# Optimization experiments

Measured on AMD Instinct MI355X. Metric: run time of the kernel, lower is better.

## Reference

```python
import jax, jax.numpy as jnp
import numpy as np

N = 50000      # nodes
E = 800000     # edges (avg degree 16)
D_IN = 128     # in_feats
D_OUT = 128    # out_feats
EPS = 1e-5     # LayerNorm eps


def setup_inputs() -> dict:
    key = jax.random.key(0)
    ks = jax.random.split(key, 8)
    stdv = 1.0 / np.sqrt(5 * D_IN)
    return {
        "h": jax.random.normal(ks[0], (N, D_IN), dtype=jnp.float32),
        "dist": jax.random.uniform(ks[1], (E,), dtype=jnp.float32),
        "W": jax.random.uniform(ks[2], (D_OUT, 5 * D_IN), minval=-stdv, maxval=stdv, dtype=jnp.float32),
        "b": jax.random.uniform(ks[3], (D_OUT,), minval=-stdv, maxval=stdv, dtype=jnp.float32),
        "gamma": jnp.ones((D_OUT,), dtype=jnp.float32),
        "beta": jnp.zeros((D_OUT,), dtype=jnp.float32),
        "src": jax.random.randint(ks[4], (E,), 0, N, dtype=jnp.int32),
        "dst": jax.random.randint(ks[5], (E,), 0, N, dtype=jnp.int32),
        "positions": jax.random.randint(ks[6], (E,), 0, 4, dtype=jnp.int32),
    }


def reference(h, dist, W, b, gamma, beta, src, dst, positions):
    n = h.shape[0]
    h_src = h[src]  # [E, D] gather once, reused by all four directions

    def direction(p):
        # edge-masked u_mul_e + sum aggregation to dst
        w = jnp.where(positions == p, dist, 0.0)
        return jax.ops.segment_sum(h_src * w[:, None], dst, num_segments=n)

    r = direction(0)   # right
    bt = direction(1)  # bottom
    l = direction(2)   # left
    t = direction(0)   # top (original code reuses positions == 0 — faithful)

    cat = jnp.concatenate([h, r, bt, l, t], axis=1)  # [N, 5D]
    z = cat @ W.T + b                                 # [N, D_OUT]
    mu = jnp.mean(z, axis=-1, keepdims=True)
    var = jnp.mean(jnp.square(z - mu), axis=-1, keepdims=True)
    z = (z - mu) * jax.lax.rsqrt(var + EPS) * gamma + beta
    return jax.nn.relu(z)
```

## Files before the change

kernel.cpp:

```cpp
#include <hip/hip_runtime.h>
#include <math.h>
#include <stdint.h>

constexpr int NN = 50000;
constexpr int EE = 800000;
constexpr int D  = 128;
constexpr int KK = 512;
constexpr int BM = 32;
constexpr int CAP = 64;
constexpr int NBLK = (NN + BM - 1) / BM;

typedef __attribute__((ext_vector_type(8)))  short bf16x8;
typedef __attribute__((ext_vector_type(16))) float f32x16;

__device__ inline unsigned short f2bf(float x) {
    unsigned u = __builtin_bit_cast(unsigned, x);
    unsigned r = (u + 0x7FFF + ((u >> 16) & 1)) >> 16;
    return (unsigned short)r;
}
__device__ inline float bf2f(unsigned short b) {
    unsigned u = ((unsigned)b) << 16;
    return __builtin_bit_cast(float, u);
}

__global__ __launch_bounds__(256) void prep_wfrag(const float* __restrict__ W,
                                                  unsigned short* __restrict__ Wfh,
                                                  unsigned short* __restrict__ Wfl)
{
    int tid = blockIdx.x * 256 + threadIdx.x;
    int ln  = tid & 31;
    int slot = (tid >> 5) & 63;
    int cb  = tid >> 11;
    int col = cb * 32 + ln;
    short h8[8], l8[8];
#pragma unroll
    for (int j = 0; j < 8; ++j) {
        int k = slot * 8 + j;
        float v = W[col * 640 + k];
        if (k >= 128 && k < 256) v += W[col * 640 + k + 384];
        unsigned short hb = f2bf(v);
        h8[j] = (short)hb;
        l8[j] = (short)f2bf(v - bf2f(hb));
    }
    *(bf16x8*)(Wfh + (size_t)tid * 8) = *(bf16x8*)h8;
    *(bf16x8*)(Wfl + (size_t)tid * 8) = *(bf16x8*)l8;
}

__global__ __launch_bounds__(256) void fill_bucket(const int* __restrict__ src,
                                                   const int* __restrict__ dst,
                                                   const int* __restrict__ pos,
                                                   const float* __restrict__ dist,
                                                   int* __restrict__ deg,
                                                   int2* __restrict__ bucket)
{
    int e = blockIdx.x * 256 + threadIdx.x;
    if (e >= EE) return;
    int p = pos[e];
    if (p == 3) return;
    int d_ = dst[e];
    int slot = atomicAdd(&deg[d_], 1);
    if (slot < CAP)
        bucket[(size_t)d_ * CAP + slot] =
            make_int2(src[e] | (p << 16), __float_as_int(dist[e]));
}

__global__ __launch_bounds__(256, 4) void fused_agg_gemm(
    const float* __restrict__ h,
    const int2* __restrict__ bucket, const int* __restrict__ deg,
    const unsigned short* __restrict__ Wfh, const unsigned short* __restrict__ Wfl,
    const float* __restrict__ bias, const float* __restrict__ gamma,
    const float* __restrict__ beta, float* __restrict__ out)
{
    __shared__ __align__(16) short Af[64 * 32 * 8];

    const int t = threadIdx.x;
    const int lane = t & 63;
    const int w = t >> 6;
    const int ln = lane & 31;
    const int hs = lane >> 5;
    const int node0 = blockIdx.x * BM;

    {
        int row = t >> 3;
        int g   = t & 7;
        int node = node0 + row;
        float ff[16];
        if (node < NN) {
            const float* hp = h + (size_t)node * D + g * 16;
            float4 f0 = *(const float4*)hp;
            float4 f1 = *(const float4*)(hp + 4);
            float4 f2 = *(const float4*)(hp + 8);
            float4 f3 = *(const float4*)(hp + 12);
            ff[0]=f0.x; ff[1]=f0.y; ff[2]=f0.z; ff[3]=f0.w;
            ff[4]=f1.x; ff[5]=f1.y; ff[6]=f1.z; ff[7]=f1.w;
            ff[8]=f2.x; ff[9]=f2.y; ff[10]=f2.z; ff[11]=f2.w;
            ff[12]=f3.x; ff[13]=f3.y; ff[14]=f3.z; ff[15]=f3.w;
        } else {
#pragma unroll
            for (int j = 0; j < 16; ++j) ff[j] = 0.f;
        }
        short b16[16];
#pragma unroll
        for (int j = 0; j < 16; ++j) b16[j] = (short)f2bf(ff[j]);
        int s0 = 2 * g, s1 = 2 * g + 1;
        *(bf16x8*)(Af + (s0 * 32 + (row ^ s0)) * 8) = *(bf16x8*)&b16[0];
        *(bf16x8*)(Af + (s1 * 32 + (row ^ s1)) * 8) = *(bf16x8*)&b16[8];
    }

    const int c0 = ln * 4;
    for (int i = 0; i < 8; ++i) {
        int r = w * 8 + i;
        int node = node0 + r;
        int n = 0;
        if (node < NN) {
            n = deg[node];
            if (n > CAP) n = CAP;
        }
        int2 mreg = (lane < n) ? bucket[(size_t)node * CAP + lane]
                               : make_int2(0, 0);

        float a0[4] = {0.f, 0.f, 0.f, 0.f};
        float a1[4] = {0.f, 0.f, 0.f, 0.f};
        float a2[4] = {0.f, 0.f, 0.f, 0.f};

        for (int base = 0; base < n; base += 16) {
            float4 v[8];
            float  wq[8];
            int    pq[8];
#pragma unroll
            for (int j = 0; j < 8; ++j) {
                int idx = base + 2 * j + hs;
                bool pred = idx < n;
                int mx = __shfl(mreg.x, idx & 63, 64);
                int my = __shfl(mreg.y, idx & 63, 64);
                pq[j] = mx >> 16;
                wq[j] = pred ? __int_as_float(my) : 0.f;
                const float* hp = h + (size_t)(mx & 0xFFFF) * D + c0;
                v[j] = pred ? *(const float4*)hp : make_float4(0.f,0.f,0.f,0.f);
            }
#pragma unroll
            for (int j = 0; j < 8; ++j) {
                float w0 = (pq[j] == 0) ? wq[j] : 0.f;
                float w1 = (pq[j] == 1) ? wq[j] : 0.f;
                float w2 = (pq[j] == 2) ? wq[j] : 0.f;
                float vv[4] = {v[j].x, v[j].y, v[j].z, v[j].w};
#pragma unroll
                for (int c = 0; c < 4; ++c) {
                    a0[c] = fmaf(vv[c], w0, a0[c]);
                    a1[c] = fmaf(vv[c], w1, a1[c]);
                    a2[c] = fmaf(vv[c], w2, a2[c]);
                }
            }
        }
#pragma unroll
        for (int c = 0; c < 4; ++c) {
            a0[c] += __shfl_xor(a0[c], 32, 64);
            a1[c] += __shfl_xor(a1[c], 32, 64);
            a2[c] += __shfl_xor(a2[c], 32, 64);
        }
        int sb = ln >> 1;
        int bo = (ln & 1) * 4;
        if (hs == 0) {
            uint2 u0 = make_uint2((unsigned)f2bf(a0[0]) | ((unsigned)f2bf(a0[1]) << 16),
                                  (unsigned)f2bf(a0[2]) | ((unsigned)f2bf(a0[3]) << 16));
            uint2 u1 = make_uint2((unsigned)f2bf(a1[0]) | ((unsigned)f2bf(a1[1]) << 16),
                                  (unsigned)f2bf(a1[2]) | ((unsigned)f2bf(a1[3]) << 16));
            int s = 16 + sb;
            *(uint2*)(Af + (s * 32 + (r ^ (s & 31))) * 8 + bo) = u0;
            s = 32 + sb;
            *(uint2*)(Af + (s * 32 + (r ^ (s & 31))) * 8 + bo) = u1;
        } else {
            uint2 u2 = make_uint2((unsigned)f2bf(a2[0]) | ((unsigned)f2bf(a2[1]) << 16),
                                  (unsigned)f2bf(a2[2]) | ((unsigned)f2bf(a2[3]) << 16));
            int s = 48 + sb;
            *(uint2*)(Af + (s * 32 + (r ^ (s & 31))) * 8 + bo) = u2;
        }
    }

    __syncthreads();

    f32x16 acc;
#pragma unroll
    for (int i = 0; i < 16; ++i) acc[i] = 0.f;

    auto LOADB = [&](int k16, bf16x8& bh, bf16x8& bl) {
        size_t fo = ((size_t)(w * 64 + k16 * 2 + hs) * 32 + ln) * 8;
        bh = *(const bf16x8*)(Wfh + fo);
        bl = *(const bf16x8*)(Wfl + fo);
    };
    auto LOADA = [&](int k16) -> bf16x8 {
        int s = k16 * 2 + hs;
        return *(const bf16x8*)(Af + (s * 32 + (ln ^ (s & 31))) * 8);
    };

    bf16x8 bh0, bl0, bh1, bl1;
    LOADB(0, bh0, bl0);
#pragma unroll
    for (int k16 = 0; k16 < 32; k16 += 2) {
        if (k16 + 1 < 32) LOADB(k16 + 1, bh1, bl1);
        bf16x8 aa = LOADA(k16);
        __builtin_amdgcn_s_setprio(1);
        acc = __builtin_amdgcn_mfma_f32_32x32x16_bf16(aa, bh0, acc, 0, 0, 0);
        acc = __builtin_amdgcn_mfma_f32_32x32x16_bf16(aa, bl0, acc, 0, 0, 0);
        __builtin_amdgcn_s_setprio(0);
        if (k16 + 2 < 32) LOADB(k16 + 2, bh0, bl0);
        aa = LOADA(k16 + 1);
        __builtin_amdgcn_s_setprio(1);
        acc = __builtin_amdgcn_mfma_f32_32x32x16_bf16(aa, bh1, acc, 0, 0, 0);
        acc = __builtin_amdgcn_mfma_f32_32x32x16_bf16(aa, bl1, acc, 0, 0, 0);
        __builtin_amdgcn_s_setprio(0);
    }

    __syncthreads();

    float* part = (float*)Af;
    float bias_c = bias[w * 32 + ln];

#pragma unroll
    for (int reg = 0; reg < 16; ++reg) {
        float z = acc[reg] + bias_c;
        acc[reg] = z;
        float s = z, ss = z * z;
#pragma unroll
        for (int m = 1; m < 32; m <<= 1) {
            s  += __shfl_xor(s, m, 64);
            ss += __shfl_xor(ss, m, 64);
        }
        int rl = (reg & 3) + 8 * (reg >> 2) + 4 * hs;
        if (ln == 0) {
            part[(w * 32 + rl) * 2]     = s;
            part[(w * 32 + rl) * 2 + 1] = ss;
        }
    }
    __syncthreads();

    float g_c  = gamma[w * 32 + ln];
    float be_c = beta[w * 32 + ln];
#pragma unroll
    for (int reg = 0; reg < 16; ++reg) {
        int rl = (reg & 3) + 8 * (reg >> 2) + 4 * hs;
        float s  = part[rl * 2]     + part[(32 + rl) * 2]
                 + part[(64 + rl) * 2] + part[(96 + rl) * 2];
        float ss = part[rl * 2 + 1] + part[(32 + rl) * 2 + 1]
                 + part[(64 + rl) * 2 + 1] + part[(96 + rl) * 2 + 1];
        float mu  = s * (1.f / 128.f);
        float var = ss * (1.f / 128.f) - mu * mu;
        float rs  = rsqrtf(var + 1e-5f);
        int grow = node0 + rl;
        if (grow < NN) {
            float v = (acc[reg] - mu) * rs * g_c + be_c;
            out[(size_t)grow * D + w * 32 + ln] = v > 0.f ? v : 0.f;
        }
    }
}

extern "C" void kernel_launch(void* const* d_in, const int* in_sizes, int n_in,
                              void* d_out, int out_size, void* d_ws, size_t ws_size,
                              hipStream_t stream)
{
    const float* h     = (const float*)d_in[0];
    const float* dist  = (const float*)d_in[1];
    const float* W     = (const float*)d_in[2];
    const float* bias  = (const float*)d_in[3];
    const float* gamma = (const float*)d_in[4];
    const float* beta  = (const float*)d_in[5];
    const int*   src   = (const int*)d_in[6];
    const int*   dst   = (const int*)d_in[7];
    const int*   pos   = (const int*)d_in[8];

    unsigned short* Wfh = (unsigned short*)d_ws;
    unsigned short* Wfl = Wfh + 128 * KK;
    int*  deg    = (int*)(Wfl + 128 * KK);
    int2* bucket = (int2*)(((uintptr_t)(deg + NN) + 15) & ~(uintptr_t)15);

    hipMemsetAsync(deg, 0, NN * sizeof(int), stream);

    prep_wfrag<<<32, 256, 0, stream>>>(W, Wfh, Wfl);
    fill_bucket<<<(EE + 255) / 256, 256, 0, stream>>>(src, dst, pos, dist, deg, bucket);
    fused_agg_gemm<<<NBLK, 256, 0, stream>>>(h, bucket, deg, Wfh, Wfl,
                                             bias, gamma, beta, (float*)d_out);
}
```

Before: 199.2 us.

## Reorder to transform-then-aggregate: project node features first, gather bf16 projections

Uses linearity to apply the per-direction weight slices to every node before aggregation: a GEMM computes the self term plus three 128-wide projections per node (stored as bf16 in Y), and a separate per-node kernel gathers the projected rows weighted by dist and applies LayerNorm/ReLU. Edge indices now encode src*3+p so each edge reads exactly one 128-wide bf16 row instead of a float row accumulated into three buffers, which halves gather bytes and cuts FMA work. In exchange it writes and rereads a 50000x384 bf16 intermediate plus a float base array, adds a kernel launch, and rounds the aggregated operand to bf16 before summation, which changes numerical error.

```diff
diff --git a/kernel.cpp b/kernel.cpp
--- a/kernel.cpp
+++ b/kernel.cpp
@@ -5,10 +5,9 @@
 constexpr int NN = 50000;
 constexpr int EE = 800000;
 constexpr int D  = 128;
-constexpr int KK = 512;
+constexpr int CAP = 64;
 constexpr int BM = 32;
-constexpr int CAP = 64;
-constexpr int NBLK = (NN + BM - 1) / BM;
+constexpr int NBX = (NN + BM - 1) / BM;
 
 typedef __attribute__((ext_vector_type(8)))  short bf16x8;
 typedef __attribute__((ext_vector_type(16))) float f32x16;
@@ -29,15 +28,20 @@
 {
     int tid = blockIdx.x * 256 + threadIdx.x;
     int ln  = tid & 31;
-    int slot = (tid >> 5) & 63;
-    int cb  = tid >> 11;
-    int col = cb * 32 + ln;
+    int hs  = (tid >> 5) & 1;
+    int s   = (tid >> 6) & 7;
+    int vcb = tid >> 9;
+    int oc  = vcb * 32 + ln;
     short h8[8], l8[8];
 #pragma unroll
     for (int j = 0; j < 8; ++j) {
-        int k = slot * 8 + j;
-        float v = W[col * 640 + k];
-        if (k >= 128 && k < 256) v += W[col * 640 + k + 384];
+        int k = s * 16 + hs * 8 + j;
+        float v;
+        if (oc < 128)      v = W[oc * 640 + k];
+        else if (oc < 256) v = W[(oc - 128) * 640 + 128 + k]
+                             + W[(oc - 128) * 640 + 512 + k];
+        else if (oc < 384) v = W[(oc - 256) * 640 + 256 + k];
+        else               v = W[(oc - 384) * 640 + 384 + k];
         unsigned short hb = f2bf(v);
         h8[j] = (short)hb;
         l8[j] = (short)f2bf(v - bf2f(hb));
@@ -61,17 +65,16 @@
     int slot = atomicAdd(&deg[d_], 1);
     if (slot < CAP)
         bucket[(size_t)d_ * CAP + slot] =
-            make_int2(src[e] | (p << 16), __float_as_int(dist[e]));
-}
-
-__global__ __launch_bounds__(256, 4) void fused_agg_gemm(
+            make_int2(src[e] * 3 + p, __float_as_int(dist[e]));
+}
+
+__global__ __launch_bounds__(256, 4) void pre_gemm(
     const float* __restrict__ h,
-    const int2* __restrict__ bucket, const int* __restrict__ deg,
     const unsigned short* __restrict__ Wfh, const unsigned short* __restrict__ Wfl,
-    const float* __restrict__ bias, const float* __restrict__ gamma,
-    const float* __restrict__ beta, float* __restrict__ out)
-{
-    __shared__ __align__(16) short Af[64 * 32 * 8];
+    const float* __restrict__ bias,
+    float* __restrict__ base, unsigned short* __restrict__ Y)
+{
+    __shared__ __align__(16) short Af[16 * 32 * 8];
 
     const int t = threadIdx.x;
     const int lane = t & 63;
@@ -79,6 +82,7 @@
     const int ln = lane & 31;
     const int hs = lane >> 5;
     const int node0 = blockIdx.x * BM;
+    const int by = blockIdx.y;
 
     {
         int row = t >> 3;
@@ -106,151 +110,121 @@
         *(bf16x8*)(Af + (s0 * 32 + (row ^ s0)) * 8) = *(bf16x8*)&b16[0];
         *(bf16x8*)(Af + (s1 * 32 + (row ^ s1)) * 8) = *(bf16x8*)&b16[8];
     }
-
-    const int c0 = ln * 4;
-    for (int i = 0; i < 8; ++i) {
-        int r = w * 8 + i;
-        int node = node0 + r;
-        int n = 0;
-        if (node < NN) {
-            n = deg[node];
-            if (n > CAP) n = CAP;
-        }
-        int2 mreg = (lane < n) ? bucket[(size_t)node * CAP + lane]
-                               : make_int2(0, 0);
-
-        float a0[4] = {0.f, 0.f, 0.f, 0.f};
-        float a1[4] = {0.f, 0.f, 0.f, 0.f};
-        float a2[4] = {0.f, 0.f, 0.f, 0.f};
-
-        for (int base = 0; base < n; base += 16) {
-            float4 v[8];
-            float  wq[8];
-            int    pq[8];
-#pragma unroll
-            for (int j = 0; j < 8; ++j) {
-                int idx = base + 2 * j + hs;
-                bool pred = idx < n;
-                int mx = __shfl(mreg.x, idx & 63, 64);
-                int my = __shfl(mreg.y, idx & 63, 64);
-                pq[j] = mx >> 16;
-                wq[j] = pred ? __int_as_float(my) : 0.f;
-                const float* hp = h + (size_t)(mx & 0xFFFF) * D + c0;
-                v[j] = pred ? *(const float4*)hp : make_float4(0.f,0.f,0.f,0.f);
-            }
-#pragma unroll
-            for (int j = 0; j < 8; ++j) {
-                float w0 = (pq[j] == 0) ? wq[j] : 0.f;
-                float w1 = (pq[j] == 1) ? wq[j] : 0.f;
-                float w2 = (pq[j] == 2) ? wq[j] : 0.f;
-                float vv[4] = {v[j].x, v[j].y, v[j].z, v[j].w};
-#pragma unroll
-                for (int c = 0; c < 4; ++c) {
-                    a0[c] = fmaf(vv[c], w0, a0[c]);
-                    a1[c] = fmaf(vv[c], w1, a1[c]);
-                    a2[c] = fmaf(vv[c], w2, a2[c]);
-                }
-            }
-        }
-#pragma unroll
-        for (int c = 0; c < 4; ++c) {
-            a0[c] += __shfl_xor(a0[c], 32, 64);
-            a1[c] += __shfl_xor(a1[c], 32, 64);
-            a2[c] += __shfl_xor(a2[c], 32, 64);
-        }
-        int sb = ln >> 1;
-        int bo = (ln & 1) * 4;
-        if (hs == 0) {
-            uint2 u0 = make_uint2((unsigned)f2bf(a0[0]) | ((unsigned)f2bf(a0[1]) << 16),
-                                  (unsigned)f2bf(a0[2]) | ((unsigned)f2bf(a0[3]) << 16));
-            uint2 u1 = make_uint2((unsigned)f2bf(a1[0]) | ((unsigned)f2bf(a1[1]) << 16),
-                                  (unsigned)f2bf(a1[2]) | ((unsigned)f2bf(a1[3]) << 16));
-            int s = 16 + sb;
-            *(uint2*)(Af + (s * 32 + (r ^ (s & 31))) * 8 + bo) = u0;
-            s = 32 + sb;
-            *(uint2*)(Af + (s * 32 + (r ^ (s & 31))) * 8 + bo) = u1;
-        } else {
-            uint2 u2 = make_uint2((unsigned)f2bf(a2[0]) | ((unsigned)f2bf(a2[1]) << 16),
-                                  (unsigned)f2bf(a2[2]) | ((unsigned)f2bf(a2[3]) << 16));
-            int s = 48 + sb;
-            *(uint2*)(Af + (s * 32 + (r ^ (s & 31))) * 8 + bo) = u2;
-        }
-    }
-
     __syncthreads();
 
-    f32x16 acc;
-#pragma unroll
-    for (int i = 0; i < 16; ++i) acc[i] = 0.f;
-
-    auto LOADB = [&](int k16, bf16x8& bh, bf16x8& bl) {
-        size_t fo = ((size_t)(w * 64 + k16 * 2 + hs) * 32 + ln) * 8;
+    const int vcb = by * 4 + w;
+
+    auto LOADB = [&](int s, bf16x8& bh, bf16x8& bl) {
+        size_t fo = ((size_t)((vcb * 8 + s) * 2 + hs) * 32 + ln) * 8;
         bh = *(const bf16x8*)(Wfh + fo);
         bl = *(const bf16x8*)(Wfl + fo);
     };
-    auto LOADA = [&](int k16) -> bf16x8 {
-        int s = k16 * 2 + hs;
-        return *(const bf16x8*)(Af + (s * 32 + (ln ^ (s & 31))) * 8);
+    auto LOADA = [&](int s) -> bf16x8 {
+        int sl = s * 2 + hs;
+        return *(const bf16x8*)(Af + (sl * 32 + (ln ^ sl)) * 8);
     };
+
+    f32x16 acc;
+#pragma unroll
+    for (int i = 0; i < 16; ++i) acc[i] = 0.f;
 
     bf16x8 bh0, bl0, bh1, bl1;
     LOADB(0, bh0, bl0);
 #pragma unroll
-    for (int k16 = 0; k16 < 32; k16 += 2) {
-        if (k16 + 1 < 32) LOADB(k16 + 1, bh1, bl1);
-        bf16x8 aa = LOADA(k16);
+    for (int s = 0; s < 8; s += 2) {
+        if (s + 1 < 8) LOADB(s + 1, bh1, bl1);
+        bf16x8 aa = LOADA(s);
         __builtin_amdgcn_s_setprio(1);
         acc = __builtin_amdgcn_mfma_f32_32x32x16_bf16(aa, bh0, acc, 0, 0, 0);
         acc = __builtin_amdgcn_mfma_f32_32x32x16_bf16(aa, bl0, acc, 0, 0, 0);
         __builtin_amdgcn_s_setprio(0);
-        if (k16 + 2 < 32) LOADB(k16 + 2, bh0, bl0);
-        aa = LOADA(k16 + 1);
+        if (s + 2 < 8) LOADB(s + 2, bh0, bl0);
+        aa = LOADA(s + 1);
         __builtin_amdgcn_s_setprio(1);
         acc = __builtin_amdgcn_mfma_f32_32x32x16_bf16(aa, bh1, acc, 0, 0, 0);
         acc = __builtin_amdgcn_mfma_f32_32x32x16_bf16(aa, bl1, acc, 0, 0, 0);
         __builtin_amdgcn_s_setprio(0);
     }
 
-    __syncthreads();
-
-    float* part = (float*)Af;
-    float bias_c = bias[w * 32 + ln];
-
-#pragma unroll
-    for (int reg = 0; reg < 16; ++reg) {
-        float z = acc[reg] + bias_c;
-        acc[reg] = z;
-        float s = z, ss = z * z;
-#pragma unroll
-        for (int m = 1; m < 32; m <<= 1) {
-            s  += __shfl_xor(s, m, 64);
-            ss += __shfl_xor(ss, m, 64);
-        }
-        int rl = (reg & 3) + 8 * (reg >> 2) + 4 * hs;
-        if (ln == 0) {
-            part[(w * 32 + rl) * 2]     = s;
-            part[(w * 32 + rl) * 2 + 1] = ss;
-        }
-    }
-    __syncthreads();
-
-    float g_c  = gamma[w * 32 + ln];
-    float be_c = beta[w * 32 + ln];
+    int vc = by * 128 + w * 32 + ln;
 #pragma unroll
     for (int reg = 0; reg < 16; ++reg) {
         int rl = (reg & 3) + 8 * (reg >> 2) + 4 * hs;
-        float s  = part[rl * 2]     + part[(32 + rl) * 2]
-                 + part[(64 + rl) * 2] + part[(96 + rl) * 2];
-        float ss = part[rl * 2 + 1] + part[(32 + rl) * 2 + 1]
-                 + part[(64 + rl) * 2 + 1] + part[(96 + rl) * 2 + 1];
-        float mu  = s * (1.f / 128.f);
-        float var = ss * (1.f / 128.f) - mu * mu;
-        float rs  = rsqrtf(var + 1e-5f);
         int grow = node0 + rl;
         if (grow < NN) {
-            float v = (acc[reg] - mu) * rs * g_c + be_c;
-            out[(size_t)grow * D + w * 32 + ln] = v > 0.f ? v : 0.f;
-        }
+            if (by == 0)
+                base[(size_t)grow * D + vc] = acc[reg] + bias[vc];
+            else
+                Y[(size_t)grow * 384 + (vc - 128)] = f2bf(acc[reg]);
+        }
+    }
+}
+
+__global__ __launch_bounds__(256, 8) void agg_ln(
+    const unsigned short* __restrict__ Y, const float* __restrict__ base,
+    const int2* __restrict__ bucket, const int* __restrict__ deg,
+    const float* __restrict__ gamma, const float* __restrict__ beta,
+    float* __restrict__ out)
+{
+    int w = threadIdx.x >> 6;
+    int node = blockIdx.x * 4 + w;
+    if (node >= NN) return;
+    int lane = threadIdx.x & 63;
+    int ln = lane & 31;
+    int hs = lane >> 5;
+
+    int n = deg[node];
+    if (n > CAP) n = CAP;
+    int2 mreg = (lane < n) ? bucket[(size_t)node * CAP + lane] : make_int2(0, 0);
+
+    float a[4] = {0.f, 0.f, 0.f, 0.f};
+    for (int b0 = 0; b0 < n; b0 += 16) {
+        ushort4 v[8];
+        float   wq[8];
+#pragma unroll
+        for (int j = 0; j < 8; ++j) {
+            int idx = b0 + 2 * j + hs;
+            int s3 = __shfl(mreg.x, idx, 64);
+            int wy = __shfl(mreg.y, idx, 64);
+            wq[j] = __int_as_float(wy);
+            v[j] = *(const ushort4*)(Y + (size_t)s3 * D + ln * 4);
+        }
+#pragma unroll
+        for (int j = 0; j < 8; ++j) {
+            a[0] = fmaf(bf2f(v[j].x), wq[j], a[0]);
+            a[1] = fmaf(bf2f(v[j].y), wq[j], a[1]);
+            a[2] = fmaf(bf2f(v[j].z), wq[j], a[2]);
+            a[3] = fmaf(bf2f(v[j].w), wq[j], a[3]);
+        }
+    }
+#pragma unroll
+    for (int c = 0; c < 4; ++c) a[c] += __shfl_xor(a[c], 32, 64);
+
+    float4 bv = *(const float4*)(base + (size_t)node * D + ln * 4);
+    float z[4] = {bv.x + a[0], bv.y + a[1], bv.z + a[2], bv.w + a[3]};
+
+    float s = z[0] + z[1] + z[2] + z[3];
+    float ss = z[0]*z[0] + z[1]*z[1] + z[2]*z[2] + z[3]*z[3];
+#pragma unroll
+    for (int m = 1; m < 32; m <<= 1) {
+        s  += __shfl_xor(s, m, 64);
+        ss += __shfl_xor(ss, m, 64);
+    }
+    float mu  = s * (1.f / 128.f);
+    float var = ss * (1.f / 128.f) - mu * mu;
+    float rs  = rsqrtf(var + 1e-5f);
+
+    if (hs == 0) {
+        float4 g4 = *(const float4*)(gamma + ln * 4);
+        float4 b4 = *(const float4*)(beta + ln * 4);
+        float o[4];
+        o[0] = (z[0] - mu) * rs * g4.x + b4.x;
+        o[1] = (z[1] - mu) * rs * g4.y + b4.y;
+        o[2] = (z[2] - mu) * rs * g4.z + b4.z;
+        o[3] = (z[3] - mu) * rs * g4.w + b4.w;
+#pragma unroll
+        for (int c = 0; c < 4; ++c) o[c] = o[c] > 0.f ? o[c] : 0.f;
+        *(float4*)(out + (size_t)node * D + ln * 4) = *(float4*)o;
     }
 }
 
@@ -268,15 +242,18 @@
     const int*   dst   = (const int*)d_in[7];
     const int*   pos   = (const int*)d_in[8];
 
-    unsigned short* Wfh = (unsigned short*)d_ws;
-    unsigned short* Wfl = Wfh + 128 * KK;
-    int*  deg    = (int*)(Wfl + 128 * KK);
+    unsigned short* Wfh  = (unsigned short*)d_ws;
+    unsigned short* Wfl  = Wfh + 8192 * 8;
+    unsigned short* Y    = Wfl + 8192 * 8;
+    float*          base = (float*)(Y + (size_t)NN * 384);
+    int*            deg  = (int*)(base + (size_t)NN * D);
     int2* bucket = (int2*)(((uintptr_t)(deg + NN) + 15) & ~(uintptr_t)15);
 
     hipMemsetAsync(deg, 0, NN * sizeof(int), stream);
 
     prep_wfrag<<<32, 256, 0, stream>>>(W, Wfh, Wfl);
     fill_bucket<<<(EE + 255) / 256, 256, 0, stream>>>(src, dst, pos, dist, deg, bucket);
-    fused_agg_gemm<<<NBLK, 256, 0, stream>>>(h, bucket, deg, Wfh, Wfl,
-                                             bias, gamma, beta, (float*)d_out);
-}
+    pre_gemm<<<dim3(NBX, 4), 256, 0, stream>>>(h, Wfh, Wfl, bias, base, Y);
+    agg_ln<<<(NN + 3) / 4, 256, 0, stream>>>(Y, base, bucket, deg, gamma, beta,
+                                             (float*)d_out);
+}
```

New measurement: 190.9 us. 1.04x faster.
